# Performance work log

Hardware: AMD Instinct MI355X
Metric: run time of the kernel (lower is better)

## Reference

```python
import jax, jax.numpy as jnp
import numpy as np

B, L, D, N_HEADS = 8, 512, 1024, 16
D_HEAD = D // N_HEADS


def _mha_fuzzy(x_q, x_k, x_v, Wq, bq, Wk, bk, Wv, bv, Wo, bo):
    """Multi-head fuzzy attention, product t-norm score function."""
    b, lq, d_model = x_q.shape
    lk = x_k.shape[1]

    def proj(x, W, bias, l):
        # [b, l, D] -> [b, h, l, d_head]
        return (x @ W + bias).reshape(b, l, N_HEADS, D_HEAD).transpose(0, 2, 1, 3)

    Q = proj(x_q, Wq, bq, lq)
    K = proj(x_k, Wk, bk, lk)
    V = proj(x_v, Wv, bv, lk)
    # fuzzy memberships in [0,1]
    mu_q = jax.nn.sigmoid(Q)
    mu_k = jax.nn.sigmoid(K)
    # product t-norm aggregated over feature dim (mean), then softmax normalize
    scores = jnp.einsum('bhid,bhjd->bhij', mu_q, mu_k) / D_HEAD  # [b,h,lq,lk]
    attn = jax.nn.softmax(scores, axis=-1)
    out = jnp.einsum('bhij,bhjd->bhid', attn, V)
    out = out.transpose(0, 2, 1, 3).reshape(b, lq, d_model)
    return out @ Wo + bo, attn.mean(axis=1)  # avg over heads


def setup_inputs() -> dict:
    key = jax.random.key(0)
    ks = jax.random.split(key, 16)
    s = 1.0 / np.sqrt(D)
    inp = {
        'text_features': jax.random.normal(ks[0], (B, L, D), jnp.float32),
        'image_features': jax.random.normal(ks[1], (B, L, D), jnp.float32),
        'Wq': jax.random.normal(ks[2], (D, D), jnp.float32) * s,
        'bq': jnp.zeros((D,), jnp.float32),
        'Wk': jax.random.normal(ks[3], (D, D), jnp.float32) * s,
        'bk': jnp.zeros((D,), jnp.float32),
        'Wv': jax.random.normal(ks[4], (D, D), jnp.float32) * s,
        'bv': jnp.zeros((D,), jnp.float32),
        'Wo': jax.random.normal(ks[5], (D, D), jnp.float32) * s,
        'bo': jnp.zeros((D,), jnp.float32),
        'W1': jax.random.normal(ks[6], (3 * D, D), jnp.float32) * (1.0 / np.sqrt(3 * D)),
        'b1': jnp.zeros((D,), jnp.float32),
        'W2': jax.random.normal(ks[7], (D, D), jnp.float32) * s,
        'b2': jnp.zeros((D,), jnp.float32),
    }
    return inp


def reference(text_features, image_features, Wq, bq, Wk, bk, Wv, bv, Wo, bo, W1, b1, W2, b2):
    # shared fuzzy attention module applied in both cross-modal directions
    text_cross, avg_attn = _mha_fuzzy(text_features, image_features, image_features,
                                      Wq, bq, Wk, bk, Wv, bv, Wo, bo)
    image_cross, _ = _mha_fuzzy(image_features, text_features, text_features,
                                Wq, bq, Wk, bk, Wv, bv, Wo, bo)
    combined = jnp.concatenate([text_features, image_features, text_cross], axis=-1)
    hidden = jax.nn.relu(combined @ W1 + b1)
    compositional_output = hidden @ W2 + b2
    return text_cross, image_cross, compositional_output, avg_attn
```

## Files before the change

### kernel.cpp

```cpp
#include <hip/hip_runtime.h>

#define NB 8
#define SL 512
#define DM 1024
#define NH 16
#define DH 64

using bfrag = __attribute__((ext_vector_type(8))) short;
using facc  = __attribute__((ext_vector_type(4))) float;

__device__ __forceinline__ float bf2f(ushort u) {
    return __uint_as_float(((unsigned)u) << 16);
}
__device__ __forceinline__ ushort f2bf(float f) {
    unsigned x = __float_as_uint(f);
    return (ushort)((x + 0x7FFFu + ((x >> 16) & 1u)) >> 16);
}
__device__ __forceinline__ float4 bf4_f4(ushort4 u) {
    return make_float4(bf2f(u.x), bf2f(u.y), bf2f(u.z), bf2f(u.w));
}
__device__ __forceinline__ unsigned pack2(float a, float b) {
    return (unsigned)f2bf(a) | ((unsigned)f2bf(b) << 16);
}
__device__ __forceinline__ void gload16(const ushort* g, ushort* l) {
    __builtin_amdgcn_global_load_lds(
        (const __attribute__((address_space(1))) unsigned*)g,
        (__attribute__((address_space(3))) unsigned*)l, 16, 0, 0);
}

__global__ __launch_bounds__(256)
void cvt_k(const float* __restrict__ s, ushort* __restrict__ d) {
    const size_t i = (size_t)(blockIdx.x * 256 + threadIdx.x) * 4;
    const float4 f = *(const float4*)(s + i);
    *(ushort4*)(d + i) = make_ushort4(f2bf(f.x), f2bf(f.y), f2bf(f.z), f2bf(f.w));
}

__global__ __launch_bounds__(256)
void tconv_k(const float* __restrict__ W, ushort* __restrict__ WT,
             const int R, const int C) {
    __shared__ ushort T[64][68];
    const int tid = threadIdx.x;
    const int c0 = blockIdx.x * 64, r0 = blockIdx.y * 64;
    #pragma unroll
    for (int rr = 0; rr < 4; ++rr) {
        const int r = (tid >> 4) + rr * 16;
        const int c4 = (tid & 15) * 4;
        const float4 f = *(const float4*)(W + (size_t)(r0 + r) * C + c0 + c4);
        T[c4+0][r] = f2bf(f.x); T[c4+1][r] = f2bf(f.y);
        T[c4+2][r] = f2bf(f.z); T[c4+3][r] = f2bf(f.w);
    }
    __syncthreads();
    #pragma unroll
    for (int rr = 0; rr < 4; ++rr) {
        const int c = (tid >> 4) + rr * 16;
        const int r4 = (tid & 15) * 4;
        *(ushort4*)(WT + (size_t)(c0 + c) * R + r0 + r4) =
            make_ushort4(T[c][r4+0], T[c][r4+1], T[c][r4+2], T[c][r4+3]);
    }
}

template<int ACT, int OMODE>
__global__ __launch_bounds__(256, 2)
void mfma_gemm(const ushort* __restrict__ A0, const ushort* __restrict__ A1,
               const float* __restrict__ A2f,
               const int KA1, const int KA2, const int Ktot,
               const int lda, const int ldaf,
               const ushort* __restrict__ AM1, const int Msplit,
               const ushort* __restrict__ BT, const int ldb,
               const float* __restrict__ bias, const float* __restrict__ biasK,
               const float* __restrict__ biasV,
               float* __restrict__ outf, ushort* __restrict__ outb,
               ushort* __restrict__ outbK, ushort* __restrict__ outbVT,
               const int clustN)
{
    __shared__ ushort sh[32768];
    const int tid  = threadIdx.x;
    const int w    = tid >> 6;
    const int lane = tid & 63;
    const int ln   = lane & 15, qd = lane >> 4;
    const int wm = (w & 1) * 64, wn = (w >> 1) * 64;

    const int NTg = gridDim.x, MTg = gridDim.y;
    const int L   = blockIdx.x + NTg * blockIdx.y;
    const int xcd = L & 7, sIdx = L >> 3;
    int mt, nt;
    if (clustN) { const int np = NTg >> 3; nt = xcd * np + sIdx % np; mt = sIdx / np; }
    else        { mt = xcd * (MTg >> 3) + sIdx / NTg; nt = sIdx - (sIdx / NTg) * NTg; }
    const int m0 = mt * 128, n0 = nt * 128;

    const ushort* A0u = A0; const ushort* A1u = A1; int m0A = m0;
    if (Msplit && m0 >= Msplit) { A0u = AM1; A1u = AM1; m0A = m0 - Msplit; }

    const int arow = (lane >> 3);
    const int kc8s = ((lane & 7) ^ arow) * 8;

    facc acc[4][4];
    #pragma unroll
    for (int i = 0; i < 4; ++i)
        #pragma unroll
        for (int j = 0; j < 4; ++j)
            acc[i][j] = (facc){0.f, 0.f, 0.f, 0.f};

    auto stage = [&](int k0, ushort* buf) {
        ushort* Asb = buf;
        ushort* Bsb = buf + 8192;
        #pragma unroll
        for (int t = 0; t < 4; ++t) {
            const int c = w * 4 + t;
            gload16(BT + (size_t)(n0 + c * 8 + arow) * ldb + k0 + kc8s,
                    &Bsb[c * 512]);
        }
        if (k0 < KA2) {
            const ushort* Ab; int ko;
            if (k0 < KA1) { Ab = A0u; ko = k0; }
            else          { Ab = A1u; ko = k0 - KA1; }
            #pragma unroll
            for (int t = 0; t < 4; ++t) {
                const int c = w * 4 + t;
                gload16(Ab + (size_t)(m0A + c * 8 + arow) * lda + ko + kc8s,
                        &Asb[c * 512]);
            }
        } else {
            const int ko = k0 - KA2;
            #pragma unroll
            for (int t = 0; t < 4; ++t) {
                const int c = w * 4 + t;
                const float* src = A2f + (size_t)(m0A + c * 8 + arow) * ldaf + ko + kc8s;
                const float4 f0 = *(const float4*)src;
                const float4 f1 = *(const float4*)(src + 4);
                uint4 p;
                p.x = pack2(f0.x, f0.y); p.y = pack2(f0.z, f0.w);
                p.z = pack2(f1.x, f1.y); p.w = pack2(f1.z, f1.w);
                *(uint4*)&Asb[c * 512 + lane * 8] = p;
            }
        }
    };

    stage(0, sh);
    for (int k0 = 0; k0 < Ktot; k0 += 64) {
        ushort* cur = sh + ((k0 >> 6) & 1) * 16384;
        ushort* nxt = sh + (((k0 >> 6) & 1) ^ 1) * 16384;
        __syncthreads();
        if (k0 + 64 < Ktot) stage(k0 + 64, nxt);
        ushort* Asb = cur;
        ushort* Bsb = cur + 8192;
        #pragma unroll
        for (int ks = 0; ks < 2; ++ks) {
            const int ch = (ks * 4 + qd) ^ (ln & 7);
            bfrag af[4], bfv[4];
            #pragma unroll
            for (int i = 0; i < 4; ++i)
                af[i] = *(const bfrag*)&Asb[(wm + i*16 + ln) * 64 + ch * 8];
            #pragma unroll
            for (int j = 0; j < 4; ++j)
                bfv[j] = *(const bfrag*)&Bsb[(wn + j*16 + ln) * 64 + ch * 8];
            #pragma unroll
            for (int i = 0; i < 4; ++i)
                #pragma unroll
                for (int j = 0; j < 4; ++j)
                    acc[i][j] = __builtin_amdgcn_mfma_f32_16x16x32_bf16(
                        af[i], bfv[j], acc[i][j], 0, 0, 0);
        }
    }

    if (OMODE == 4) {
        const int seg   = n0 >> 10;
        const int nloc0 = n0 & 1023;
        const float* bs = (seg == 0) ? bias : (seg == 1) ? biasK : biasV;
        if (seg < 2) {
            ushort* ob = (seg == 0) ? outb : outbK;
            #pragma unroll
            for (int j = 0; j < 4; ++j) {
                const int nl = nloc0 + wn + j * 16 + ln;
                const float bn = bs[nl];
                #pragma unroll
                for (int i = 0; i < 4; ++i) {
                    const int mb = m0 + wm + i * 16 + qd * 4;
                    #pragma unroll
                    for (int r = 0; r < 4; ++r) {
                        const float v = 1.f / (1.f + __expf(-(acc[i][j][r] + bn)));
                        const int m = mb + r;
                        const int g = m >> 9, l = m & 511;
                        ob[(((size_t)(g * NH + (nl >> 6))) * SL + l) * DH + (nl & 63)]
                            = f2bf(v);
                    }
                }
            }
        } else {
            __syncthreads();
            #pragma unroll
            for (int j = 0; j < 4; ++j) {
                const int n_l = wn + j * 16 + ln;
                const float bn = bs[nloc0 + n_l];
                #pragma unroll
                for (int i = 0; i < 4; ++i) {
                    #pragma unroll
                    for (int r = 0; r < 4; ++r) {
                        const int m_l = wm + i * 16 + qd * 4 + r;
                        const int c = (m_l >> 3) ^ (n_l & 7);
                        sh[n_l * 128 + c * 8 + (m_l & 7)] = f2bf(acc[i][j][r] + bn);
                    }
                }
            }
            __syncthreads();
            const int n_l = tid >> 1, half = tid & 1;
            const int nl = nloc0 + n_l;
            const int g = m0 >> 9, l0 = m0 & 511;
            ushort* dst = outbVT +
                (((size_t)(g * NH + (nl >> 6))) * DH + (nl & 63)) * SL + l0;
            #pragma unroll
            for (int u = 0; u < 8; ++u) {
                const int c = half * 8 + u;
                const int cs = c ^ (n_l & 7);
                *(uint4*)(dst + c * 8) = *(const uint4*)&sh[n_l * 128 + cs * 8];
            }
        }
        return;
    }

    #pragma unroll
    for (int j = 0; j < 4; ++j) {
        const int n = n0 + wn + j * 16 + ln;
        const float bn = bias[n];
        #pragma unroll
        for (int i = 0; i < 4; ++i) {
            const int mb = m0 + wm + i * 16 + qd * 4;
            #pragma unroll
            for (int r = 0; r < 4; ++r) {
                float v = acc[i][j][r] + bn;
                if (ACT == 1)      v = 1.f / (1.f + __expf(-v));
                else if (ACT == 2) v = v > 0.f ? v : 0.f;
                const int m = mb + r;
                if (OMODE == 0) outf[(size_t)m * DM + n] = v;
                else            outb[(size_t)m * DM + n] = f2bf(v);
            }
        }
    }
}

__global__ __launch_bounds__(256, 2)
void attn2_k(const ushort* __restrict__ Qm, const ushort* __restrict__ Km,
             const ushort* __restrict__ VTm, ushort* __restrict__ AO,
             float* __restrict__ RS)
{
    __shared__ ushort Ks[128 * 64];
    __shared__ ushort VTs[64 * 128];
    __shared__ ushort Es[128 * 128];
    const int tid  = threadIdx.x;
    const int w    = tid >> 6;
    const int lane = tid & 63;
    const int ln   = lane & 15, qd = lane >> 4;
    const int wm  = (w & 1) * 64;
    const int wns = (w >> 1) * 64;
    const int wnd = (w >> 1) * 32;
    const int qt = blockIdx.x, h = blockIdx.y, b = blockIdx.z;
    const size_t ho = ((size_t)(b * NH + h)) * SL * DH;
    const ushort* Qg  = Qm  + ho + (size_t)qt * 128 * DH;
    const ushort* Kg  = Km  + ho;
    const ushort* VTg = VTm + ho;

    bfrag qf[4][2];
    #pragma unroll
    for (int i = 0; i < 4; ++i)
        #pragma unroll
        for (int ks = 0; ks < 2; ++ks)
            qf[i][ks] = *(const bfrag*)(Qg + (size_t)(wm + i*16 + ln) * DH + ks*32 + qd*8);

    facc oacc[4][2];
    #pragma unroll
    for (int i = 0; i < 4; ++i)
        #pragma unroll
        for (int j = 0; j < 2; ++j)
            oacc[i][j] = (facc){0.f, 0.f, 0.f, 0.f};
    float rp[4][4];
    #pragma unroll
    for (int i = 0; i < 4; ++i)
        #pragma unroll
        for (int r = 0; r < 4; ++r)
            rp[i][r] = 0.f;

    const int arow = lane >> 3;
    const int kc8s = ((lane & 7) ^ arow) * 8;
    const int vrow = lane >> 4;

    for (int kc = 0; kc < 4; ++kc) {
        __syncthreads();
        #pragma unroll
        for (int t = 0; t < 4; ++t) {
            const int c = w * 4 + t;
            const int vc8s = ((lane & 15) ^ ((c * 4 + vrow) & 7)) * 8;
            gload16(Kg + (size_t)(kc*128 + c*8 + arow) * DH + kc8s, &Ks[c * 512]);
            gload16(VTg + (size_t)(c*4 + vrow) * SL + kc*128 + vc8s, &VTs[c * 512]);
        }
        __syncthreads();

        facc sacc[4][4];
        #pragma unroll
        for (int i = 0; i < 4; ++i)
            #pragma unroll
            for (int j = 0; j < 4; ++j)
                sacc[i][j] = (facc){0.f, 0.f, 0.f, 0.f};
        #pragma unroll
        for (int ks = 0; ks < 2; ++ks) {
            const int ch = (ks * 4 + qd) ^ (ln & 7);
            bfrag kf[4];
            #pragma unroll
            for (int j = 0; j < 4; ++j)
                kf[j] = *(const bfrag*)&Ks[(wns + j*16 + ln) * 64 + ch * 8];
            #pragma unroll
            for (int i = 0; i < 4; ++i)
                #pragma unroll
                for (int j = 0; j < 4; ++j)
                    sacc[i][j] = __builtin_amdgcn_mfma_f32_16x16x32_bf16(
                        qf[i][ks], kf[j], sacc[i][j], 0, 0, 0);
        }

        #pragma unroll
        for (int i = 0; i < 4; ++i) {
            #pragma unroll
            for (int r = 0; r < 4; ++r) {
                const int q = wm + i*16 + qd*4 + r;
                float p = 0.f;
                #pragma unroll
                for (int j = 0; j < 4; ++j) {
                    const float e = __expf(sacc[i][j][r] * 0.015625f);
                    const int key = wns + j*16 + ln;
                    const int c = (key >> 3) ^ (q & 7);
                    Es[q * 128 + c * 8 + (key & 7)] = f2bf(e);
                    p += e;
                }
                p += __shfl_xor(p, 1, 16);
                p += __shfl_xor(p, 2, 16);
                p += __shfl_xor(p, 4, 16);
                p += __shfl_xor(p, 8, 16);
                rp[i][r] += p;
            }
        }
        __syncthreads();

        #pragma unroll
        for (int ks2 = 0; ks2 < 4; ++ks2) {
            const int vch = (ks2 * 4 + qd) ^ (ln & 7);
            bfrag ea[4], vb[2];
            #pragma unroll
            for (int i = 0; i < 4; ++i) {
                const int q = wm + i*16 + ln;
                const int cs = (ks2*4 + qd) ^ (q & 7);
                ea[i] = *(const bfrag*)&Es[q * 128 + cs * 8];
            }
            #pragma unroll
            for (int j = 0; j < 2; ++j)
                vb[j] = *(const bfrag*)&VTs[(wnd + j*16 + ln) * 128 + vch * 8];
            #pragma unroll
            for (int i = 0; i < 4; ++i)
                #pragma unroll
                for (int j = 0; j < 2; ++j)
                    oacc[i][j] = __builtin_amdgcn_mfma_f32_16x16x32_bf16(
                        ea[i], vb[j], oacc[i][j], 0, 0, 0);
        }
    }

    __syncthreads();
    float* rsls = (float*)Ks;
    if (ln == 0) {
        #pragma unroll
        for (int i = 0; i < 4; ++i)
            #pragma unroll
            for (int r = 0; r < 4; ++r)
                rsls[(w >> 1) * 128 + wm + i*16 + qd*4 + r] = rp[i][r];
    }
    __syncthreads();
    if (tid < 128) {
        const float t = rsls[tid] + rsls[128 + tid];
        RS[(size_t)(b * NH + h) * SL + qt * 128 + tid] = t;
        rsls[tid] = t;
    }
    __syncthreads();

    #pragma unroll
    for (int i = 0; i < 4; ++i) {
        #pragma unroll
        for (int r = 0; r < 4; ++r) {
            const int q = wm + i*16 + qd*4 + r;
            const float inv = 1.f / rsls[q];
            const size_t rowo = ((size_t)(b*SL + qt*128 + q)) * DM + h*DH;
            #pragma unroll
            for (int j = 0; j < 2; ++j)
                AO[rowo + wnd + j*16 + ln] = f2bf(oacc[i][j][r] * inv);
        }
    }
}

__global__ __launch_bounds__(256, 2)
void avg3_k(const ushort* __restrict__ Qm, const ushort* __restrict__ Km,
            const float* __restrict__ RS, float* __restrict__ avga)
{
    __shared__ ushort Qs[64 * 64];
    __shared__ ushort Kt[64 * 64];
    __shared__ float rss[64];
    const int tid  = threadIdx.x;
    const int w    = tid >> 6;
    const int lane = tid & 63;
    const int ln   = lane & 15, qd = lane >> 4;
    const int wq = (w & 1) * 32, wk = (w >> 1) * 32;
    const int kt = blockIdx.x, qt = blockIdx.y, b = blockIdx.z;

    const int arow = lane >> 3;
    const int kc8s = ((lane & 7) ^ arow) * 8;

    float acc[2][2][4];
    #pragma unroll
    for (int i = 0; i < 2; ++i)
        #pragma unroll
        for (int j = 0; j < 2; ++j)
            #pragma unroll
            for (int r = 0; r < 4; ++r)
                acc[i][j][r] = 0.f;

    for (int h = 0; h < NH; ++h) {
        const size_t ho = ((size_t)(b * NH + h)) * SL * DH;
        __syncthreads();
        #pragma unroll
        for (int t = 0; t < 2; ++t) {
            const int c = w * 2 + t;
            gload16(Qm + ho + (size_t)(qt*64 + c*8 + arow) * DH + kc8s, &Qs[c * 512]);
            gload16(Km + ho + (size_t)(kt*64 + c*8 + arow) * DH + kc8s, &Kt[c * 512]);
        }
        if (tid < 64) rss[tid] = RS[(size_t)(b*NH + h)*SL + qt*64 + tid];
        __syncthreads();

        facc s[2][2];
        #pragma unroll
        for (int i = 0; i < 2; ++i)
            #pragma unroll
            for (int j = 0; j < 2; ++j)
                s[i][j] = (facc){0.f, 0.f, 0.f, 0.f};
        #pragma unroll
        for (int ks = 0; ks < 2; ++ks) {
            const int ch = (ks * 4 + qd) ^ (ln & 7);
            bfrag qa[2], kb[2];
            #pragma unroll
            for (int i = 0; i < 2; ++i)
                qa[i] = *(const bfrag*)&Qs[(wq + i*16 + ln) * 64 + ch * 8];
            #pragma unroll
            for (int j = 0; j < 2; ++j)
                kb[j] = *(const bfrag*)&Kt[(wk + j*16 + ln) * 64 + ch * 8];
            #pragma unroll
            for (int i = 0; i < 2; ++i)
                #pragma unroll
                for (int j = 0; j < 2; ++j)
                    s[i][j] = __builtin_amdgcn_mfma_f32_16x16x32_bf16(
                        qa[i], kb[j], s[i][j], 0, 0, 0);
        }
        #pragma unroll
        for (int i = 0; i < 2; ++i) {
            #pragma unroll
            for (int r = 0; r < 4; ++r) {
                const float ir = 0.0625f / rss[wq + i*16 + qd*4 + r];
                #pragma unroll
                for (int j = 0; j < 2; ++j)
                    acc[i][j][r] += __expf(s[i][j][r] * 0.015625f) * ir;
            }
        }
    }
    #pragma unroll
    for (int i = 0; i < 2; ++i) {
        #pragma unroll
        for (int r = 0; r < 4; ++r) {
            const int q = wq + i*16 + qd*4 + r;
            #pragma unroll
            for (int j = 0; j < 2; ++j)
                avga[((size_t)(b*SL + qt*64 + q)) * SL + kt*64 + wk + j*16 + ln]
                    = acc[i][j][r];
        }
    }
}

extern "C" void kernel_launch(void* const* d_in, const int* in_sizes, int n_in,
                              void* d_out, int out_size, void* d_ws, size_t ws_size,
                              hipStream_t stream)
{
    (void)in_sizes; (void)n_in; (void)out_size; (void)ws_size;
    const float* text  = (const float*)d_in[0];
    const float* image = (const float*)d_in[1];
    const float* Wq = (const float*)d_in[2];
    const float* bq = (const float*)d_in[3];
    const float* Wk = (const float*)d_in[4];
    const float* bk = (const float*)d_in[5];
    const float* Wv = (const float*)d_in[6];
    const float* bv = (const float*)d_in[7];
    const float* Wo = (const float*)d_in[8];
    const float* bo = (const float*)d_in[9];
    const float* W1 = (const float*)d_in[10];
    const float* b1 = (const float*)d_in[11];
    const float* W2 = (const float*)d_in[12];
    const float* b2 = (const float*)d_in[13];
    float* out = (float*)d_out;

    const size_t SZ   = (size_t)NB * SL * DM;
    const size_t HALF = SZ;

    ushort* xbf = (ushort*)d_ws;
    ushort* Qb  = xbf + 2*SZ;
    ushort* Kb  = Qb  + 2*SZ;
    ushort* VT  = Kb  + 2*SZ;
    ushort* AOt = VT  + 2*SZ;
    ushort* Wt  = AOt + SZ;
    float*  RS  = (float*)(Wt + 3*DM*DM);
    ushort* AOi    = VT + HALF;
    ushort* hidden = Qb;

    float* text_cross = out;
    float* comp       = out + 2*SZ;
    float* avga       = out + 3*SZ;

    const dim3 blk(256);

    cvt_k<<<4096, blk, 0, stream>>>(text,  xbf);
    cvt_k<<<4096, blk, 0, stream>>>(image, xbf + SZ);

    tconv_k<<<dim3(16,16), blk, 0, stream>>>(Wq, Wt,           DM, DM);
    tconv_k<<<dim3(16,16), blk, 0, stream>>>(Wk, Wt + DM*DM,   DM, DM);
    tconv_k<<<dim3(16,16), blk, 0, stream>>>(Wv, Wt + 2*DM*DM, DM, DM);
    mfma_gemm<0,4><<<dim3(24,64), blk, 0, stream>>>(
        xbf, xbf, nullptr, DM, DM, DM, DM, DM, nullptr, 0,
        Wt, DM, bq, bk, bv, nullptr, Qb, Kb, VT, 1);

    attn2_k<<<dim3(SL/128, NH, NB), blk, 0, stream>>>(Qb, Kb + HALF, VT + HALF, AOt, RS);
    avg3_k<<<dim3(SL/64, SL/64, NB), blk, 0, stream>>>(Qb, Kb + HALF, RS, avga);
    attn2_k<<<dim3(SL/128, NH, NB), blk, 0, stream>>>(Qb + HALF, Kb, VT, AOi, RS);

    tconv_k<<<dim3(16,16), blk, 0, stream>>>(Wo, Wt, DM, DM);
    mfma_gemm<0,0><<<dim3(8,64), blk, 0, stream>>>(
        AOt, AOt, nullptr, DM, DM, DM, DM, DM, AOi, 4096,
        Wt, DM, bo, nullptr, nullptr, text_cross, nullptr, nullptr, nullptr, 0);

    tconv_k<<<dim3(16,48), blk, 0, stream>>>(W1, Wt, 3*DM, DM);
    mfma_gemm<2,2><<<dim3(8,32), blk, 0, stream>>>(
        xbf, xbf + SZ, text_cross, DM, 2*DM, 3*DM, DM, DM, nullptr, 0,
        Wt, 3*DM, b1, nullptr, nullptr, nullptr, hidden, nullptr, nullptr, 0);
    tconv_k<<<dim3(16,16), blk, 0, stream>>>(W2, Wt, DM, DM);
    mfma_gemm<0,0><<<dim3(8,32), blk, 0, stream>>>(
        hidden, hidden, nullptr, DM, DM, DM, DM, DM, nullptr, 0,
        Wt, DM, b2, nullptr, nullptr, comp, nullptr, nullptr, nullptr, 0);
}
```

Before: 400.5 us.

## Double-buffer LDS staging in attention and head-averaged attention kernels

In the attention kernel, the V^T tile is now double-buffered. The K and V^T loads for the next key chunk are issued after the softmax barrier, so they overlap the PV matmul instead of sitting behind a barrier at the top of each iteration. In the head-averaging kernel, the Q, K and row-sum tiles are double-buffered per head, and the next head is prefetched while the current one is computed. This trades a larger LDS footprint (about 80KB per block in the attention kernel), which could limit occupancy, for fewer exposed global-load stalls.

Measured after the change: 428.9 us. 7.1% more time.

```diff
diff --git a/kernel.cpp b/kernel.cpp
--- a/kernel.cpp
+++ b/kernel.cpp
@@ -244,7 +244,7 @@
              float* __restrict__ RS)
 {
     __shared__ ushort Ks[128 * 64];
-    __shared__ ushort VTs[64 * 128];
+    __shared__ ushort VTs[2][64 * 128];
     __shared__ ushort Es[128 * 128];
     const int tid  = threadIdx.x;
     const int w    = tid >> 6;
@@ -283,15 +283,19 @@
     const int kc8s = ((lane & 7) ^ arow) * 8;
     const int vrow = lane >> 4;
 
-    for (int kc = 0; kc < 4; ++kc) {
-        __syncthreads();
+    auto stage = [&](int kc, ushort* vtb) {
         #pragma unroll
         for (int t = 0; t < 4; ++t) {
             const int c = w * 4 + t;
             const int vc8s = ((lane & 15) ^ ((c * 4 + vrow) & 7)) * 8;
             gload16(Kg + (size_t)(kc*128 + c*8 + arow) * DH + kc8s, &Ks[c * 512]);
-            gload16(VTg + (size_t)(c*4 + vrow) * SL + kc*128 + vc8s, &VTs[c * 512]);
-        }
+            gload16(VTg + (size_t)(c*4 + vrow) * SL + kc*128 + vc8s, &vtb[c * 512]);
+        }
+    };
+
+    stage(0, VTs[0]);
+    for (int kc = 0; kc < 4; ++kc) {
+        const int cur = kc & 1;
         __syncthreads();
 
         facc sacc[4][4];
@@ -338,6 +342,8 @@
         }
         __syncthreads();
 
+        if (kc + 1 < 4) stage(kc + 1, VTs[cur ^ 1]);
+
         #pragma unroll
         for (int ks2 = 0; ks2 < 4; ++ks2) {
             const int vch = (ks2 * 4 + qd) ^ (ln & 7);
@@ -350,7 +356,7 @@
             }
             #pragma unroll
             for (int j = 0; j < 2; ++j)
-                vb[j] = *(const bfrag*)&VTs[(wnd + j*16 + ln) * 128 + vch * 8];
+                vb[j] = *(const bfrag*)&VTs[cur][(wnd + j*16 + ln) * 128 + vch * 8];
             #pragma unroll
             for (int i = 0; i < 4; ++i)
                 #pragma unroll
@@ -395,9 +401,9 @@
 void avg3_k(const ushort* __restrict__ Qm, const ushort* __restrict__ Km,
             const float* __restrict__ RS, float* __restrict__ avga)
 {
-    __shared__ ushort Qs[64 * 64];
-    __shared__ ushort Kt[64 * 64];
-    __shared__ float rss[64];
+    __shared__ ushort Qs[2][64 * 64];
+    __shared__ ushort Kt[2][64 * 64];
+    __shared__ float rss[2][64];
     const int tid  = threadIdx.x;
     const int w    = tid >> 6;
     const int lane = tid & 63;
@@ -417,17 +423,24 @@
             for (int r = 0; r < 4; ++r)
                 acc[i][j][r] = 0.f;
 
-    for (int h = 0; h < NH; ++h) {
+    auto stageh = [&](int h, int pb) {
         const size_t ho = ((size_t)(b * NH + h)) * SL * DH;
-        __syncthreads();
         #pragma unroll
         for (int t = 0; t < 2; ++t) {
             const int c = w * 2 + t;
-            gload16(Qm + ho + (size_t)(qt*64 + c*8 + arow) * DH + kc8s, &Qs[c * 512]);
-            gload16(Km + ho + (size_t)(kt*64 + c*8 + arow) * DH + kc8s, &Kt[c * 512]);
-        }
-        if (tid < 64) rss[tid] = RS[(size_t)(b*NH + h)*SL + qt*64 + tid];
+            gload16(Qm + ho + (size_t)(qt*64 + c*8 + arow) * DH + kc8s,
+                    &Qs[pb][c * 512]);
+            gload16(Km + ho + (size_t)(kt*64 + c*8 + arow) * DH + kc8s,
+                    &Kt[pb][c * 512]);
+        }
+        if (tid < 64) rss[pb][tid] = RS[(size_t)(b*NH + h)*SL + qt*64 + tid];
+    };
+
+    stageh(0, 0);
+    for (int h = 0; h < NH; ++h) {
+        const int pb = h & 1;
         __syncthreads();
+        if (h + 1 < NH) stageh(h + 1, pb ^ 1);
 
         facc s[2][2];
         #pragma unroll
@@ -441,10 +454,10 @@
             bfrag qa[2], kb[2];
             #pragma unroll
             for (int i = 0; i < 2; ++i)
-                qa[i] = *(const bfrag*)&Qs[(wq + i*16 + ln) * 64 + ch * 8];
+                qa[i] = *(const bfrag*)&Qs[pb][(wq + i*16 + ln) * 64 + ch * 8];
             #pragma unroll
             for (int j = 0; j < 2; ++j)
-                kb[j] = *(const bfrag*)&Kt[(wk + j*16 + ln) * 64 + ch * 8];
+                kb[j] = *(const bfrag*)&Kt[pb][(wk + j*16 + ln) * 64 + ch * 8];
             #pragma unroll
             for (int i = 0; i < 2; ++i)
                 #pragma unroll
@@ -456,7 +469,7 @@
         for (int i = 0; i < 2; ++i) {
             #pragma unroll
             for (int r = 0; r < 4; ++r) {
-                const float ir = 0.0625f / rss[wq + i*16 + qd*4 + r];
+                const float ir = 0.0625f / rss[pb][wq + i*16 + qd*4 + r];
                 #pragma unroll
                 for (int j = 0; j < 2; ++j)
                     acc[i][j][r] += __expf(s[i][j][r] * 0.015625f) * ir;
```

## Merge conversion, weight transposes and both attention directions into fewer launches

Applied to the files above, without the earlier changes.

Folds the two input casts into one launch and the Q/K/V/O weight transposes into a single batched launch. Both cross-attention directions now run in one attention launch of twice the grid, with direction selected by blockIdx.z. WoT, AOi and the second row-sum buffer are placed in scratch regions of the output and workspace so both directions can run at once. The per-row sum shuffle reduction moves out of the key loop to run once at the end. The aim is to cut launch count and tail effects and let the two attention directions fill the GPU together; the cost is more aliasing of buffers that must not overlap.

Result: faster. 381.6 us (-4.7%).

```diff
diff --git a/kernel.cpp b/kernel.cpp
--- a/kernel.cpp
+++ b/kernel.cpp
@@ -16,9 +16,6 @@
     unsigned x = __float_as_uint(f);
     return (ushort)((x + 0x7FFFu + ((x >> 16) & 1u)) >> 16);
 }
-__device__ __forceinline__ float4 bf4_f4(ushort4 u) {
-    return make_float4(bf2f(u.x), bf2f(u.y), bf2f(u.z), bf2f(u.w));
-}
 __device__ __forceinline__ unsigned pack2(float a, float b) {
     return (unsigned)f2bf(a) | ((unsigned)f2bf(b) << 16);
 }
@@ -29,15 +26,19 @@
 }
 
 __global__ __launch_bounds__(256)
-void cvt_k(const float* __restrict__ s, ushort* __restrict__ d) {
+void cvt2_k(const float* __restrict__ s0, const float* __restrict__ s1,
+            ushort* __restrict__ d) {
+    const size_t half = (size_t)NB * SL * DM;
+    const float* s = blockIdx.z ? s1 : s0;
+    ushort* dd = d + (size_t)blockIdx.z * half;
     const size_t i = (size_t)(blockIdx.x * 256 + threadIdx.x) * 4;
     const float4 f = *(const float4*)(s + i);
-    *(ushort4*)(d + i) = make_ushort4(f2bf(f.x), f2bf(f.y), f2bf(f.z), f2bf(f.w));
-}
-
-__global__ __launch_bounds__(256)
-void tconv_k(const float* __restrict__ W, ushort* __restrict__ WT,
-             const int R, const int C) {
+    *(ushort4*)(dd + i) = make_ushort4(f2bf(f.x), f2bf(f.y), f2bf(f.z), f2bf(f.w));
+}
+
+__device__ __forceinline__ void tconv_body(const float* __restrict__ W,
+                                           ushort* __restrict__ WT,
+                                           const int R, const int C) {
     __shared__ ushort T[64][68];
     const int tid = threadIdx.x;
     const int c0 = blockIdx.x * 64, r0 = blockIdx.y * 64;
@@ -57,6 +58,22 @@
         *(ushort4*)(WT + (size_t)(c0 + c) * R + r0 + r4) =
             make_ushort4(T[c][r4+0], T[c][r4+1], T[c][r4+2], T[c][r4+3]);
     }
+}
+
+__global__ __launch_bounds__(256)
+void tconv_k(const float* __restrict__ W, ushort* __restrict__ WT,
+             const int R, const int C) {
+    tconv_body(W, WT, R, C);
+}
+
+__global__ __launch_bounds__(256)
+void tconv4_k(const float* __restrict__ W0, const float* __restrict__ W1,
+              const float* __restrict__ W2, const float* __restrict__ W3,
+              ushort* __restrict__ Wt012, ushort* __restrict__ WT3) {
+    const int z = blockIdx.z;
+    const float* W = (z == 0) ? W0 : (z == 1) ? W1 : (z == 2) ? W2 : W3;
+    ushort* WT = (z < 3) ? (Wt012 + (size_t)z * DM * DM) : WT3;
+    tconv_body(W, WT, DM, DM);
 }
 
 template<int ACT, int OMODE>
@@ -239,9 +256,10 @@
 }
 
 __global__ __launch_bounds__(256, 2)
-void attn2_k(const ushort* __restrict__ Qm, const ushort* __restrict__ Km,
-             const ushort* __restrict__ VTm, ushort* __restrict__ AO,
-             float* __restrict__ RS)
+void attn2m_k(const ushort* __restrict__ Qm, const ushort* __restrict__ Km,
+              const ushort* __restrict__ VTm, ushort* __restrict__ AO0,
+              ushort* __restrict__ AO1, float* __restrict__ RS0,
+              float* __restrict__ RS1)
 {
     __shared__ ushort Ks[128 * 64];
     __shared__ ushort VTs[64 * 128];
@@ -253,11 +271,20 @@
     const int wm  = (w & 1) * 64;
     const int wns = (w >> 1) * 64;
     const int wnd = (w >> 1) * 32;
-    const int qt = blockIdx.x, h = blockIdx.y, b = blockIdx.z;
+    const int qt = blockIdx.x, h = blockIdx.y;
+    const int zz = blockIdx.z;
+    const int dir = zz >> 3, b = zz & 7;
+    const size_t HALFc = (size_t)NB * SL * DM;
+    const ushort* Qall = Qm  + (dir ? HALFc : 0);
+    const ushort* Kall = Km  + (dir ? 0 : HALFc);
+    const ushort* Vall = VTm + (dir ? 0 : HALFc);
+    ushort* AOp = dir ? AO1 : AO0;
+    float*  RSp = dir ? RS1 : RS0;
+
     const size_t ho = ((size_t)(b * NH + h)) * SL * DH;
-    const ushort* Qg  = Qm  + ho + (size_t)qt * 128 * DH;
-    const ushort* Kg  = Km  + ho;
-    const ushort* VTg = VTm + ho;
+    const ushort* Qg  = Qall + ho + (size_t)qt * 128 * DH;
+    const ushort* Kg  = Kall + ho;
+    const ushort* VTg = Vall + ho;
 
     bfrag qf[4][2];
     #pragma unroll
@@ -329,10 +356,6 @@
                     Es[q * 128 + c * 8 + (key & 7)] = f2bf(e);
                     p += e;
                 }
-                p += __shfl_xor(p, 1, 16);
-                p += __shfl_xor(p, 2, 16);
-                p += __shfl_xor(p, 4, 16);
-                p += __shfl_xor(p, 8, 16);
                 rp[i][r] += p;
             }
         }
@@ -360,6 +383,19 @@
         }
     }
 
+    #pragma unroll
+    for (int i = 0; i < 4; ++i) {
+        #pragma unroll
+        for (int r = 0; r < 4; ++r) {
+            float p = rp[i][r];
+            p += __shfl_xor(p, 1, 16);
+            p += __shfl_xor(p, 2, 16);
+            p += __shfl_xor(p, 4, 16);
+            p += __shfl_xor(p, 8, 16);
+            rp[i][r] = p;
+        }
+    }
+
     __syncthreads();
     float* rsls = (float*)Ks;
     if (ln == 0) {
@@ -372,7 +408,7 @@
     __syncthreads();
     if (tid < 128) {
         const float t = rsls[tid] + rsls[128 + tid];
-        RS[(size_t)(b * NH + h) * SL + qt * 128 + tid] = t;
+        RSp[(size_t)(b * NH + h) * SL + qt * 128 + tid] = t;
         rsls[tid] = t;
     }
     __syncthreads();
@@ -386,7 +422,7 @@
             const size_t rowo = ((size_t)(b*SL + qt*128 + q)) * DM + h*DH;
             #pragma unroll
             for (int j = 0; j < 2; ++j)
-                AO[rowo + wnd + j*16 + ln] = f2bf(oacc[i][j][r] * inv);
+                AOp[rowo + wnd + j*16 + ln] = f2bf(oacc[i][j][r] * inv);
         }
     }
 }
@@ -507,33 +543,32 @@
     ushort* AOt = VT  + 2*SZ;
     ushort* Wt  = AOt + SZ;
     float*  RS  = (float*)(Wt + 3*DM*DM);
-    ushort* AOi    = VT + HALF;
     ushort* hidden = Qb;
 
     float* text_cross = out;
     float* comp       = out + 2*SZ;
     float* avga       = out + 3*SZ;
 
+    ushort* WoT = (ushort*)comp;
+    ushort* AOi = WoT + DM*DM;
+    float*  RS2 = (float*)Wt;
+
     const dim3 blk(256);
 
-    cvt_k<<<4096, blk, 0, stream>>>(text,  xbf);
-    cvt_k<<<4096, blk, 0, stream>>>(image, xbf + SZ);
-
-    tconv_k<<<dim3(16,16), blk, 0, stream>>>(Wq, Wt,           DM, DM);
-    tconv_k<<<dim3(16,16), blk, 0, stream>>>(Wk, Wt + DM*DM,   DM, DM);
-    tconv_k<<<dim3(16,16), blk, 0, stream>>>(Wv, Wt + 2*DM*DM, DM, DM);
+    cvt2_k<<<dim3(4096,1,2), blk, 0, stream>>>(text, image, xbf);
+
+    tconv4_k<<<dim3(16,16,4), blk, 0, stream>>>(Wq, Wk, Wv, Wo, Wt, WoT);
+
     mfma_gemm<0,4><<<dim3(24,64), blk, 0, stream>>>(
         xbf, xbf, nullptr, DM, DM, DM, DM, DM, nullptr, 0,
         Wt, DM, bq, bk, bv, nullptr, Qb, Kb, VT, 1);
 
-    attn2_k<<<dim3(SL/128, NH, NB), blk, 0, stream>>>(Qb, Kb + HALF, VT + HALF, AOt, RS);
+    attn2m_k<<<dim3(SL/128, NH, 16), blk, 0, stream>>>(Qb, Kb, VT, AOt, AOi, RS, RS2);
     avg3_k<<<dim3(SL/64, SL/64, NB), blk, 0, stream>>>(Qb, Kb + HALF, RS, avga);
-    attn2_k<<<dim3(SL/128, NH, NB), blk, 0, stream>>>(Qb + HALF, Kb, VT, AOi, RS);
-
-    tconv_k<<<dim3(16,16), blk, 0, stream>>>(Wo, Wt, DM, DM);
+
     mfma_gemm<0,0><<<dim3(8,64), blk, 0, stream>>>(
         AOt, AOt, nullptr, DM, DM, DM, DM, DM, AOi, 4096,
-        Wt, DM, bo, nullptr, nullptr, text_cross, nullptr, nullptr, nullptr, 0);
+        WoT, DM, bo, nullptr, nullptr, text_cross, nullptr, nullptr, nullptr, 0);
 
     tconv_k<<<dim3(16,48), blk, 0, stream>>>(W1, Wt, 3*DM, DM);
     mfma_gemm<2,2><<<dim3(8,32), blk, 0, stream>>>(
```
